# Performance work log

Hardware: AMD Instinct MI355X
Metric: run time of the kernel (lower is better)

The kernel has to match this reference:

```python
import jax, jax.numpy as jnp
import numpy as np

VOCAB, EMBED, ENC, DEC, ATT = 10000, 256, 2048, 512, 512
B, P, T = 64, 49, 30


def setup_inputs() -> dict:
    key = jax.random.key(0)
    ks = jax.random.split(key, 20)
    s = 0.02
    emb = jax.random.normal(ks[0], (VOCAB, EMBED), jnp.float32) * s
    emb = emb.at[0].set(0.0)  # padding_idx=0
    inp = {
        'features': jax.random.normal(ks[1], (B, P, ENC), jnp.float32),
        'captions': jax.random.randint(ks[2], (B, T), 0, VOCAB),
        'emb': emb,
        'W1': jax.random.normal(ks[3], (ATT, ENC), jnp.float32) * s,
        'b1': jnp.zeros((ATT,), jnp.float32),
        'W2': jax.random.normal(ks[4], (ATT, DEC), jnp.float32) * s,
        'b2': jnp.zeros((ATT,), jnp.float32),
        'V': jax.random.normal(ks[5], (1, ATT), jnp.float32) * s,
        'bV': jnp.zeros((1,), jnp.float32),
        'W_ih1': jax.random.normal(ks[6], (4 * DEC, EMBED + ENC), jnp.float32) * s,
        'W_hh1': jax.random.normal(ks[7], (4 * DEC, DEC), jnp.float32) * s,
        'b_ih1': jnp.zeros((4 * DEC,), jnp.float32),
        'b_hh1': jnp.zeros((4 * DEC,), jnp.float32),
        'W_ih2': jax.random.normal(ks[8], (4 * DEC, DEC), jnp.float32) * s,
        'W_hh2': jax.random.normal(ks[9], (4 * DEC, DEC), jnp.float32) * s,
        'b_ih2': jnp.zeros((4 * DEC,), jnp.float32),
        'b_hh2': jnp.zeros((4 * DEC,), jnp.float32),
        'fc_W': jax.random.normal(ks[10], (VOCAB, DEC), jnp.float32) * s,
        'fc_b': jnp.zeros((VOCAB,), jnp.float32),
    }
    return inp


def _lstm_cell(x, h, c, Wih, Whh, bih, bhh):
    g = x @ Wih.T + bih + h @ Whh.T + bhh  # [B, 4D]
    i, f, gg, o = jnp.split(g, 4, axis=-1)  # PyTorch gate order i,f,g,o
    c_new = jax.nn.sigmoid(f) * c + jax.nn.sigmoid(i) * jnp.tanh(gg)
    h_new = jax.nn.sigmoid(o) * jnp.tanh(c_new)
    return h_new, c_new


def reference(features, captions, emb, W1, b1, W2, b2, V, bV,
              W_ih1, W_hh1, b_ih1, b_hh1, W_ih2, W_hh2, b_ih2, b_hh2,
              fc_W, fc_b):
    # dropout is identity (eval mode / deterministic reference)
    batch = features.shape[0]
    dec = W_hh1.shape[1]
    feat_W1 = jnp.einsum('bpe,ae->bpa', features, W1) + b1  # precompute W1(features)
    embs = emb[captions]  # [B, T, E]

    def step(carry, x_t):
        h1, c1, h2, c2 = carry
        # Bahdanau attention with hidden state h2
        att = jnp.tanh(feat_W1 + (h2 @ W2.T + b2)[:, None, :])  # [B, P, A]
        score = att @ V.T + bV  # [B, P, 1]
        w = jax.nn.softmax(score, axis=1)
        ctx = jnp.sum(w * features, axis=1)  # [B, ENC]
        lstm_in = jnp.concatenate([x_t, ctx], axis=1)
        h1n, c1n = _lstm_cell(lstm_in, h1, c1, W_ih1, W_hh1, b_ih1, b_hh1)
        h2n, c2n = _lstm_cell(h1n, h2, c2, W_ih2, W_hh2, b_ih2, b_hh2)
        out = h2n @ fc_W.T + fc_b  # [B, V]
        return (h1n, c1n, h2n, c2n), out

    init = tuple(jnp.zeros((batch, dec), features.dtype) for _ in range(4))
    _, outs = jax.lax.scan(step, init, jnp.swapaxes(embs, 0, 1))  # [T, B, V]
    return jnp.swapaxes(outs, 0, 1)  # [B, T, V]
```

## Files before the change

kernel.cpp:

```cpp
#include <hip/hip_runtime.h>
#include <math.h>

#define VOCAB 10000
#define VPAD  10240
#define EMBED 256
#define ENC   2048
#define DEC   512
#define ATT   512
#define B_    64
#define P_    49
#define T_    30
#define G4    2048
#define SL    32768

typedef __bf16 bf16_t;
typedef bf16_t bf16x8 __attribute__((ext_vector_type(8)));
typedef float  f32x4  __attribute__((ext_vector_type(4)));

__device__ __forceinline__ float sigf(float x) { return 1.f / (1.f + expf(-x)); }

__global__ void prep_k(
    const float* __restrict__ b_ih1, const float* __restrict__ b_hh1, float* __restrict__ bsum1,
    const float* __restrict__ b_ih2, const float* __restrict__ b_hh2, float* __restrict__ bsum2,
    const float* __restrict__ W2,    bf16_t* __restrict__ W2sp,
    const float* __restrict__ W_hh1, bf16_t* __restrict__ fp1h,
    const float* __restrict__ W_ih2, const float* __restrict__ W_hh2, bf16_t* __restrict__ fp2,
    const float* __restrict__ fc_W,  bf16_t* __restrict__ fcWb,
    const int* __restrict__ caps, const float* __restrict__ emb, bf16_t* __restrict__ xgb,
    bf16_t* __restrict__ h1s0, bf16_t* __restrict__ h2s0,
    float* __restrict__ c1s0, float* __restrict__ c2s0,
    float* __restrict__ hwp, float* __restrict__ G1h)
{
    long stride = (long)gridDim.x * blockDim.x;
    long i0 = (long)blockIdx.x * blockDim.x + threadIdx.x;
    for (long i = i0; i < SL; i += stride) {
        h1s0[i] = (bf16_t)0.f; h2s0[i] = (bf16_t)0.f;
        c1s0[i] = 0.f; c2s0[i] = 0.f;
    }
    for (long i = i0; i < 32L * SL; i += stride) hwp[i] = 0.f;
    for (long i = i0; i < 64L * 2048; i += stride) G1h[i] = 0.f;
    for (long i = i0; i < 2048; i += stride) {
        bsum1[i] = b_ih1[i] + b_hh1[i];
        bsum2[i] = b_ih2[i] + b_hh2[i];
    }
    for (long i = i0; i < 32L * 32 * 64 * 8; i += stride) {
        long j8 = i & 7, lq = (i >> 3) & 63, nt = (i >> 9) & 31, nb = i >> 14;
        long k = (lq >> 4) * 8 + j8;
        long a = nt * 16 + (lq & 15);
        W2sp[i] = (bf16_t)(k < 16 ? W2[a * 512 + nb * 16 + k] : 0.f);
    }
    for (long i = i0; i < 32L * 16 * 2048; i += stride) {
        long j8 = i & 7, lq = (i >> 3) & 63, s = (i >> 9) & 3, nk = i >> 11;
        long kf = nk & 15, nb = nk >> 4;
        long c = s * 512 + nb * 16 + (lq & 15);
        long k = kf * 32 + (lq >> 4) * 8 + j8;
        fp1h[i] = (bf16_t)W_hh1[c * 512 + k];
    }
    for (long i = i0; i < 2048L * 1024; i += stride) {
        long j8 = i & 7, lq = (i >> 3) & 63, s = (i >> 9) & 3, nk = i >> 11;
        long kf = nk & 31, nb = nk >> 5;
        long c = s * 512 + nb * 16 + (lq & 15);
        long k = kf * 32 + (lq >> 4) * 8 + j8;
        fp2[i] = (bf16_t)(k < 512 ? W_ih2[c * 512 + k] : W_hh2[c * 512 + (k - 512)]);
    }
    for (long i = i0; i < (long)VPAD * 512; i += stride) {
        long r = i >> 9;
        fcWb[i] = (bf16_t)(r < VOCAB ? fc_W[i] : 0.f);
    }
    for (long i = i0; i < 1920L * 256; i += stride) {
        long row = i >> 8, e = i & 255;
        long tq = row >> 6, b = row & 63;
        int cap = caps[b * T_ + tq];
        xgb[i] = (bf16_t)emb[(long)cap * 256 + e];
    }
}

__global__ __launch_bounds__(256) void mm3_k(
    const float* __restrict__ features, const bf16_t* __restrict__ xgb,
    const float* __restrict__ W1, const float* __restrict__ W_ih1,
    const float* __restrict__ b1, const float* __restrict__ bsum1,
    bf16_t* __restrict__ fW1b, bf16_t* __restrict__ xembb, bf16_t* __restrict__ F1g)
{
    int bid = blockIdx.x;
    const float* Af; const bf16_t* Ab = nullptr; int lda;
    const float* Bw; int ldb, boff;
    const float* bias; bf16_t* outB; int ldo, K, bn, bm;
    if (bid < 392) {
        Af = features; lda = ENC; Bw = W1; ldb = ENC; boff = 0;
        bias = b1; outB = fW1b; ldo = ATT; K = ENC;
        bn = (bid & 7) * 64; bm = (bid >> 3) * 64;
    } else if (bid < 1352) {
        int b2i = bid - 392;
        Af = nullptr; Ab = xgb; lda = EMBED; Bw = W_ih1; ldb = EMBED + ENC; boff = 0;
        bias = bsum1; outB = xembb; ldo = G4; K = EMBED;
        bn = (b2i & 31) * 64; bm = (b2i >> 5) * 64;
    } else {
        int b3i = bid - 1352;
        Af = features; lda = ENC; Bw = W_ih1; ldb = EMBED + ENC; boff = EMBED;
        bias = nullptr; outB = F1g; ldo = G4; K = ENC;
        bn = (b3i & 31) * 64; bm = (b3i >> 5) * 64;
    }

    __shared__ bf16_t Apad[64][72];
    __shared__ bf16_t Bpad[64][72];
    const int tid = threadIdx.x;
    const int w = tid >> 6, l = tid & 63;
    f32x4 acc[4] = {};

    for (int k0 = 0; k0 < K; k0 += 64) {
        for (int c = tid; c < 512; c += 256) {
            int row = c >> 3, q = c & 7;
            if (Af) {
                const float* as = &Af[(size_t)(bm + row) * lda + k0 + q * 8];
                float4 f0 = *(const float4*)as;
                float4 f1 = *(const float4*)(as + 4);
                bf16x8 v;
                v[0] = (bf16_t)f0.x; v[1] = (bf16_t)f0.y; v[2] = (bf16_t)f0.z; v[3] = (bf16_t)f0.w;
                v[4] = (bf16_t)f1.x; v[5] = (bf16_t)f1.y; v[6] = (bf16_t)f1.z; v[7] = (bf16_t)f1.w;
                *(bf16x8*)&Apad[row][q * 8] = v;
            } else {
                *(bf16x8*)&Apad[row][q * 8] = *(const bf16x8*)&Ab[(size_t)(bm + row) * lda + k0 + q * 8];
            }
            const float* bs = &Bw[(size_t)(bn + row) * ldb + boff + k0 + q * 8];
            float4 f0 = *(const float4*)bs;
            float4 f1 = *(const float4*)(bs + 4);
            bf16x8 v;
            v[0] = (bf16_t)f0.x; v[1] = (bf16_t)f0.y; v[2] = (bf16_t)f0.z; v[3] = (bf16_t)f0.w;
            v[4] = (bf16_t)f1.x; v[5] = (bf16_t)f1.y; v[6] = (bf16_t)f1.z; v[7] = (bf16_t)f1.w;
            *(bf16x8*)&Bpad[row][q * 8] = v;
        }
        __syncthreads();
#pragma unroll
        for (int ks = 0; ks < 2; ++ks) {
            bf16x8 a8 = *(const bf16x8*)&Apad[w * 16 + (l & 15)][ks * 32 + (l >> 4) * 8];
#pragma unroll
            for (int nf = 0; nf < 4; ++nf) {
                bf16x8 b8 = *(const bf16x8*)&Bpad[nf * 16 + (l & 15)][ks * 32 + (l >> 4) * 8];
                acc[nf] = __builtin_amdgcn_mfma_f32_16x16x32_bf16(a8, b8, acc[nf], 0, 0, 0);
            }
        }
        __syncthreads();
    }

    int rbase = bm + w * 16 + (l >> 4) * 4;
    int cl = l & 15;
#pragma unroll
    for (int nf = 0; nf < 4; ++nf) {
        int col = bn + nf * 16 + cl;
        float bv = bias ? bias[col] : 0.f;
#pragma unroll
        for (int j = 0; j < 4; ++j)
            outB[(size_t)(rbase + j) * ldo + col] = (bf16_t)(acc[nf][j] + bv);
    }
}

__global__ __launch_bounds__(256) void mm_fc(
    const bf16_t* __restrict__ A, int lda,
    const bf16_t* __restrict__ Bw, int ldb,
    const float* __restrict__ bias,
    float* __restrict__ outF, int ldo, int N, int K)
{
    __shared__ bf16_t Apad[64][72];
    __shared__ bf16_t Bpad[64][72];
    const int bn = blockIdx.x * 64, bm = blockIdx.y * 64;
    const int tid = threadIdx.x;
    const int w = tid >> 6, l = tid & 63;
    f32x4 acc[4] = {};

    for (int k0 = 0; k0 < K; k0 += 64) {
        for (int c = tid; c < 512; c += 256) {
            int row = c >> 3, q = c & 7;
            *(bf16x8*)&Apad[row][q * 8] = *(const bf16x8*)&A[(size_t)(bm + row) * lda + k0 + q * 8];
            *(bf16x8*)&Bpad[row][q * 8] = *(const bf16x8*)&Bw[(size_t)(bn + row) * ldb + k0 + q * 8];
        }
        __syncthreads();
#pragma unroll
        for (int ks = 0; ks < 2; ++ks) {
            bf16x8 a8 = *(const bf16x8*)&Apad[w * 16 + (l & 15)][ks * 32 + (l >> 4) * 8];
#pragma unroll
            for (int nf = 0; nf < 4; ++nf) {
                bf16x8 b8 = *(const bf16x8*)&Bpad[nf * 16 + (l & 15)][ks * 32 + (l >> 4) * 8];
                acc[nf] = __builtin_amdgcn_mfma_f32_16x16x32_bf16(a8, b8, acc[nf], 0, 0, 0);
            }
        }
        __syncthreads();
    }

    int rbase = bm + w * 16 + (l >> 4) * 4;
    int cl = l & 15;
#pragma unroll
    for (int nf = 0; nf < 4; ++nf) {
        int col = bn + nf * 16 + cl;
#pragma unroll
        for (int j = 0; j < 4; ++j) {
            int row = rbase + j;
            if (col < N) {
                int orow = (row & 63) * T_ + (row >> 6);
                outF[(size_t)orow * ldo + col] = acc[nf][j] + bias[col];
            }
        }
    }
}

__global__ __launch_bounds__(512) void attn1_k(
    const float* __restrict__ hwp, const float* __restrict__ b2,
    const bf16_t* __restrict__ fW1b, const float* __restrict__ V,
    const float* __restrict__ bV, const bf16_t* __restrict__ F1g,
    const bf16_t* __restrict__ xeb, const float* __restrict__ G1h,
    const float* __restrict__ c1r, float* __restrict__ c1w,
    bf16_t* __restrict__ h1w)
{
    const int b = blockIdx.x, tid = threadIdx.x;
    const int w = tid >> 6, l = tid & 63;
    __shared__ float hw[512];
    __shared__ float sc[64];
    __shared__ float wn[64];
    __shared__ float gsum[2][2048];

    {
        float a0 = b2[tid];
        const float* hp = hwp + (size_t)b * 16384 + tid;
#pragma unroll 8
        for (int nb = 0; nb < 32; ++nb) a0 += hp[nb * 512];
        hw[tid] = a0;
    }
    __syncthreads();
    {
        float hwr[8], Vr[8];
#pragma unroll
        for (int i = 0; i < 8; ++i) { hwr[i] = hw[l * 8 + i]; Vr[i] = V[l * 8 + i]; }
        for (int pq = w; pq < P_; pq += 8) {
            bf16x8 f8 = *(const bf16x8*)&fW1b[(size_t)(b * P_ + pq) * 512 + l * 8];
            float s = 0.f;
#pragma unroll
            for (int i = 0; i < 8; ++i) s += tanhf((float)f8[i] + hwr[i]) * Vr[i];
#pragma unroll
            for (int o = 32; o; o >>= 1) s += __shfl_xor(s, o);
            if (l == 0) sc[pq] = s + bV[0];
        }
    }
    __syncthreads();
    {
        float m = -1e30f;
        for (int q = 0; q < P_; ++q) m = fmaxf(m, sc[q]);
        float ss = 0.f;
        for (int q = 0; q < P_; ++q) ss += expf(sc[q] - m);
        if (tid < P_) wn[tid] = expf(sc[tid] - m) / ss;
    }
    __syncthreads();
    {
        const int h = tid >> 8, th = tid & 255;
        const int p0 = h ? 25 : 0, pn = h ? 24 : 25;
        float acc[8] = {};
        const bf16_t* fg = F1g + ((size_t)b * P_ + p0) * 2048 + th * 8;
        for (int q = 0; q < pn; ++q) {
            bf16x8 f8 = *(const bf16x8*)&fg[(size_t)q * 2048];
            float wq = wn[p0 + q];
#pragma unroll
            for (int i = 0; i < 8; ++i) acc[i] += wq * (float)f8[i];
        }
#pragma unroll
        for (int i = 0; i < 8; ++i) gsum[h][th * 8 + i] = acc[i];
    }
    __syncthreads();
    {
        const int d = tid;
        const bf16_t* xb = xeb + (size_t)b * G4;
        const float* gh = G1h + b * 2048;
        float gi = (float)xb[d]        + gsum[0][d]        + gsum[1][d]        + gh[d];
        float gf = (float)xb[512 + d]  + gsum[0][512 + d]  + gsum[1][512 + d]  + gh[512 + d];
        float gg = (float)xb[1024 + d] + gsum[0][1024 + d] + gsum[1][1024 + d] + gh[1024 + d];
        float go = (float)xb[1536 + d] + gsum[0][1536 + d] + gsum[1][1536 + d] + gh[1536 + d];
        int idx = b * 512 + d;
        float cn = sigf(gf) * c1r[idx] + sigf(gi) * tanhf(gg);
        c1w[idx] = cn;
        h1w[idx] = (bf16_t)(sigf(go) * tanhf(cn));
    }
}

__global__ __launch_bounds__(512) void gate2_k(
    const bf16_t* __restrict__ h1n, const bf16_t* __restrict__ h2r,
    const bf16_t* __restrict__ fp2, const bf16_t* __restrict__ fp1h,
    const bf16_t* __restrict__ W2sp, const float* __restrict__ bsum2,
    const float* __restrict__ c2r, float* __restrict__ c2w,
    bf16_t* __restrict__ h2w, float* __restrict__ G1h, float* __restrict__ hwp)
{
    const int bid = blockIdx.x, tid = threadIdx.x;
    const int w = tid >> 6, l = tid & 63;
    const int l15 = l & 15, koff = (l >> 4) * 8;
    const int mt = w & 3, kh = w >> 2;
    __shared__ float red[2][4][4][256];
    __shared__ bf16_t h2t[64 * 16];

    if (bid < 32) {
        const int nb = bid;
        {
            const int arow = mt * 16 + l15;
            const bf16_t* ap = (kh == 0 ? h1n : h2r) + arow * 512 + koff;
            const bf16_t* wp = fp2 + ((size_t)nb * 32 + kh * 16) * 2048 + l * 8;
            f32x4 acc[4] = {};
#pragma unroll
            for (int kf = 0; kf < 16; ++kf) {
                bf16x8 a8 = *(const bf16x8*)&ap[kf * 32];
                const bf16_t* wk = wp + (size_t)kf * 2048;
#pragma unroll
                for (int s = 0; s < 4; ++s) {
                    bf16x8 w8 = *(const bf16x8*)&wk[s * 512];
                    acc[s] = __builtin_amdgcn_mfma_f32_16x16x32_bf16(a8, w8, acc[s], 0, 0, 0);
                }
            }
#pragma unroll
            for (int s = 0; s < 4; ++s) *(f32x4*)&red[kh][mt][s][l * 4] = acc[s];
        }
        __syncthreads();
        if (w < 4) {
            const int d = nb * 16 + l15;
            const int rb = w * 16 + ((l >> 4) << 2);
            f32x4 v[4];
#pragma unroll
            for (int s = 0; s < 4; ++s)
                v[s] = *(const f32x4*)&red[0][w][s][l * 4] + *(const f32x4*)&red[1][w][s][l * 4];
#pragma unroll
            for (int j = 0; j < 4; ++j) {
                int row = rb + j;
                float gi = v[0][j] + bsum2[d];
                float gf = v[1][j] + bsum2[512 + d];
                float gg = v[2][j] + bsum2[1024 + d];
                float go = v[3][j] + bsum2[1536 + d];
                float cn = sigf(gf) * c2r[row * 512 + d] + sigf(gi) * tanhf(gg);
                c2w[row * 512 + d] = cn;
                bf16_t hb = (bf16_t)(sigf(go) * tanhf(cn));
                h2w[row * 512 + d] = hb;
                h2t[row * 16 + l15] = hb;
            }
        }
        __syncthreads();
        {
            bf16x8 a8 = {};
            if ((l >> 4) < 2) a8 = *(const bf16x8*)&h2t[(mt * 16 + l15) * 16 + koff];
            const int row0 = mt * 16 + (l >> 4) * 4;
            for (int q = 0; q < 16; ++q) {
                int nt = kh * 16 + q;
                bf16x8 b8 = *(const bf16x8*)&W2sp[((size_t)(nb * 32 + nt) * 64 + l) * 8];
                f32x4 acc2 = {};
                acc2 = __builtin_amdgcn_mfma_f32_16x16x32_bf16(a8, b8, acc2, 0, 0, 0);
                const int col = nt * 16 + l15;
#pragma unroll
                for (int j = 0; j < 4; ++j)
                    hwp[(size_t)(row0 + j) * 16384 + nb * 512 + col] = acc2[j];
            }
        }
    } else {
        const int nb = bid - 32;
        {
            const int arow = mt * 16 + l15;
            const bf16_t* ap = h1n + arow * 512 + kh * 256 + koff;
            const bf16_t* wp = fp1h + ((size_t)nb * 16 + kh * 8) * 2048 + l * 8;
            f32x4 acc[4] = {};
#pragma unroll
            for (int kf = 0; kf < 8; ++kf) {
                bf16x8 a8 = *(const bf16x8*)&ap[kf * 32];
                const bf16_t* wk = wp + (size_t)kf * 2048;
#pragma unroll
                for (int s = 0; s < 4; ++s) {
                    bf16x8 w8 = *(const bf16x8*)&wk[s * 512];
                    acc[s] = __builtin_amdgcn_mfma_f32_16x16x32_bf16(a8, w8, acc[s], 0, 0, 0);
                }
            }
#pragma unroll
            for (int s = 0; s < 4; ++s) *(f32x4*)&red[kh][mt][s][l * 4] = acc[s];
        }
        __syncthreads();
        if (w < 4) {
            const int d = nb * 16 + l15;
            const int rb = w * 16 + ((l >> 4) << 2);
#pragma unroll
            for (int s = 0; s < 4; ++s) {
                f32x4 v = *(const f32x4*)&red[0][w][s][l * 4] + *(const f32x4*)&red[1][w][s][l * 4];
#pragma unroll
                for (int j = 0; j < 4; ++j)
                    G1h[(rb + j) * 2048 + s * 512 + d] = v[j];
            }
        }
    }
}

extern "C" void kernel_launch(void* const* d_in, const int* in_sizes, int n_in,
                              void* d_out, int out_size, void* d_ws, size_t ws_size,
                              hipStream_t stream)
{
    const float* features = (const float*)d_in[0];
    const int*   captions = (const int*)d_in[1];
    const float* emb   = (const float*)d_in[2];
    const float* W1    = (const float*)d_in[3];
    const float* b1    = (const float*)d_in[4];
    const float* W2    = (const float*)d_in[5];
    const float* b2    = (const float*)d_in[6];
    const float* V     = (const float*)d_in[7];
    const float* bV    = (const float*)d_in[8];
    const float* W_ih1 = (const float*)d_in[9];
    const float* W_hh1 = (const float*)d_in[10];
    const float* b_ih1 = (const float*)d_in[11];
    const float* b_hh1 = (const float*)d_in[12];
    const float* W_ih2 = (const float*)d_in[13];
    const float* W_hh2 = (const float*)d_in[14];
    const float* b_ih2 = (const float*)d_in[15];
    const float* b_hh2 = (const float*)d_in[16];
    const float* fc_W  = (const float*)d_in[17];
    const float* fc_b  = (const float*)d_in[18];
    float* out = (float*)d_out;

    char* ws = (char*)d_ws;
    size_t off = 0;
    auto alloc = [&](size_t nbytes) {
        char* pp = ws + off;
        off = (off + nbytes + 255) & ~(size_t)255;
        return pp;
    };
    bf16_t* fW1b   = (bf16_t*)alloc(3136L * 512 * 2);
    bf16_t* F1g    = (bf16_t*)alloc(3136L * 2048 * 2);
    bf16_t* W2sp   = (bf16_t*)alloc(32L * 32 * 64 * 8 * 2);
    bf16_t* fp1h   = (bf16_t*)alloc(32L * 16 * 2048 * 2);
    bf16_t* fp2    = (bf16_t*)alloc(2048L * 1024 * 2);
    bf16_t* fcWb   = (bf16_t*)alloc((size_t)VPAD * 512 * 2);
    bf16_t* xgb    = (bf16_t*)alloc(1920L * 256 * 2);
    bf16_t* xembb  = (bf16_t*)alloc(1920L * 2048 * 2);
    float*  bsum1  = (float*)alloc(2048 * 4);
    float*  bsum2  = (float*)alloc(2048 * 4);
    float*  hwp    = (float*)alloc(32L * SL * 4);
    float*  G1h    = (float*)alloc(64L * 2048 * 4);
    bf16_t* h1s    = (bf16_t*)alloc((size_t)(T_ + 1) * SL * 2);
    bf16_t* h2s    = (bf16_t*)alloc((size_t)(T_ + 1) * SL * 2);
    float*  c1s    = (float*)alloc(2L * SL * 4);
    float*  c2s    = (float*)alloc(2L * SL * 4);

    prep_k<<<4096, 256, 0, stream>>>(
        b_ih1, b_hh1, bsum1, b_ih2, b_hh2, bsum2,
        W2, W2sp, W_hh1, fp1h, W_ih2, W_hh2, fp2, fc_W, fcWb,
        captions, emb, xgb,
        h1s, h2s, c1s, c2s, hwp, G1h);

    mm3_k<<<2920, 256, 0, stream>>>(
        features, xgb, W1, W_ih1, b1, bsum1, fW1b, xembb, F1g);

    for (int t = 0; t < T_; ++t) {
        attn1_k<<<B_, 512, 0, stream>>>(
            hwp, b2, fW1b, V, bV, F1g,
            xembb + (size_t)t * B_ * G4, G1h,
            c1s + (size_t)(t & 1) * SL, c1s + (size_t)((t + 1) & 1) * SL,
            h1s + (size_t)(t + 1) * SL);
        gate2_k<<<64, 512, 0, stream>>>(
            h1s + (size_t)(t + 1) * SL, h2s + (size_t)t * SL,
            fp2, fp1h, W2sp, bsum2,
            c2s + (size_t)(t & 1) * SL, c2s + (size_t)((t + 1) & 1) * SL,
            h2s + (size_t)(t + 1) * SL, G1h, hwp);
    }

    mm_fc<<<dim3(VPAD / 64, (T_ * B_) / 64), 256, 0, stream>>>(
        h2s + SL, DEC, fcWb, DEC, fc_b, out, VOCAB, VOCAB, DEC);
}
```

Baseline: 1.140 ms.

## Fuse prep and input GEMM kernels into one launch with gathered embeddings

Merges the preprocessing kernel and the three-segment input GEMM kernel into a single launch. Extra blocks beyond the GEMM tiles do the zeroing, bias sums and weight repacking. The embedding gather now happens inside the GEMM A-tile load, so the xgb buffer goes away, and the layer-1 bias sum is computed in the epilogue instead of in prep. This removes one launch and the serialization between prep and GEMM, letting the two run concurrently, at the cost of uncoalesced gathered embedding loads.

Measured after the change: 1.146 ms. No clear change (+0.5%).

```diff
diff --git a/kernel.cpp b/kernel.cpp
--- a/kernel.cpp
+++ b/kernel.cpp
@@ -12,6 +12,8 @@
 #define T_    30
 #define G4    2048
 #define SL    32768
+#define NGEMM 2920
+#define NPREP 1080
 
 typedef __bf16 bf16_t;
 typedef bf16_t bf16x8 __attribute__((ext_vector_type(8)));
@@ -19,107 +21,101 @@
 
 __device__ __forceinline__ float sigf(float x) { return 1.f / (1.f + expf(-x)); }
 
-__global__ void prep_k(
-    const float* __restrict__ b_ih1, const float* __restrict__ b_hh1, float* __restrict__ bsum1,
-    const float* __restrict__ b_ih2, const float* __restrict__ b_hh2, float* __restrict__ bsum2,
-    const float* __restrict__ W2,    bf16_t* __restrict__ W2sp,
-    const float* __restrict__ W_hh1, bf16_t* __restrict__ fp1h,
-    const float* __restrict__ W_ih2, const float* __restrict__ W_hh2, bf16_t* __restrict__ fp2,
-    const float* __restrict__ fc_W,  bf16_t* __restrict__ fcWb,
-    const int* __restrict__ caps, const float* __restrict__ emb, bf16_t* __restrict__ xgb,
-    bf16_t* __restrict__ h1s0, bf16_t* __restrict__ h2s0,
-    float* __restrict__ c1s0, float* __restrict__ c2s0,
-    float* __restrict__ hwp, float* __restrict__ G1h)
+struct MegaP {
+    const float *features, *emb, *W1, *b1, *W2, *W_ih1, *W_hh1, *W_ih2, *W_hh2;
+    const float *b_ih1, *b_hh1, *b_ih2, *b_hh2, *fc_W;
+    const int* caps;
+    bf16_t *fW1b, *xembb, *F1g, *W2sp, *fp1h, *fp2, *fcWb;
+    float *bsum2, *hwp, *G1h, *c1s0, *c2s0;
+    bf16_t *h1s0, *h2s0;
+};
+
+__global__ __launch_bounds__(256) void mega_k(MegaP p)
 {
-    long stride = (long)gridDim.x * blockDim.x;
-    long i0 = (long)blockIdx.x * blockDim.x + threadIdx.x;
-    for (long i = i0; i < SL; i += stride) {
-        h1s0[i] = (bf16_t)0.f; h2s0[i] = (bf16_t)0.f;
-        c1s0[i] = 0.f; c2s0[i] = 0.f;
-    }
-    for (long i = i0; i < 32L * SL; i += stride) hwp[i] = 0.f;
-    for (long i = i0; i < 64L * 2048; i += stride) G1h[i] = 0.f;
-    for (long i = i0; i < 2048; i += stride) {
-        bsum1[i] = b_ih1[i] + b_hh1[i];
-        bsum2[i] = b_ih2[i] + b_hh2[i];
-    }
-    for (long i = i0; i < 32L * 32 * 64 * 8; i += stride) {
-        long j8 = i & 7, lq = (i >> 3) & 63, nt = (i >> 9) & 31, nb = i >> 14;
-        long k = (lq >> 4) * 8 + j8;
-        long a = nt * 16 + (lq & 15);
-        W2sp[i] = (bf16_t)(k < 16 ? W2[a * 512 + nb * 16 + k] : 0.f);
-    }
-    for (long i = i0; i < 32L * 16 * 2048; i += stride) {
-        long j8 = i & 7, lq = (i >> 3) & 63, s = (i >> 9) & 3, nk = i >> 11;
-        long kf = nk & 15, nb = nk >> 4;
-        long c = s * 512 + nb * 16 + (lq & 15);
-        long k = kf * 32 + (lq >> 4) * 8 + j8;
-        fp1h[i] = (bf16_t)W_hh1[c * 512 + k];
-    }
-    for (long i = i0; i < 2048L * 1024; i += stride) {
-        long j8 = i & 7, lq = (i >> 3) & 63, s = (i >> 9) & 3, nk = i >> 11;
-        long kf = nk & 31, nb = nk >> 5;
-        long c = s * 512 + nb * 16 + (lq & 15);
-        long k = kf * 32 + (lq >> 4) * 8 + j8;
-        fp2[i] = (bf16_t)(k < 512 ? W_ih2[c * 512 + k] : W_hh2[c * 512 + (k - 512)]);
-    }
-    for (long i = i0; i < (long)VPAD * 512; i += stride) {
-        long r = i >> 9;
-        fcWb[i] = (bf16_t)(r < VOCAB ? fc_W[i] : 0.f);
-    }
-    for (long i = i0; i < 1920L * 256; i += stride) {
-        long row = i >> 8, e = i & 255;
-        long tq = row >> 6, b = row & 63;
-        int cap = caps[b * T_ + tq];
-        xgb[i] = (bf16_t)emb[(long)cap * 256 + e];
-    }
-}
-
-__global__ __launch_bounds__(256) void mm3_k(
-    const float* __restrict__ features, const bf16_t* __restrict__ xgb,
-    const float* __restrict__ W1, const float* __restrict__ W_ih1,
-    const float* __restrict__ b1, const float* __restrict__ bsum1,
-    bf16_t* __restrict__ fW1b, bf16_t* __restrict__ xembb, bf16_t* __restrict__ F1g)
-{
-    int bid = blockIdx.x;
-    const float* Af; const bf16_t* Ab = nullptr; int lda;
+    const int bid = blockIdx.x;
+    const int tid = threadIdx.x;
+
+    if (bid >= NGEMM) {
+        long stride = (long)NPREP * 256;
+        long i0 = (long)(bid - NGEMM) * 256 + tid;
+        for (long i = i0; i < SL; i += stride) {
+            p.h1s0[i] = (bf16_t)0.f; p.h2s0[i] = (bf16_t)0.f;
+            p.c1s0[i] = 0.f; p.c2s0[i] = 0.f;
+        }
+        for (long i = i0; i < 32L * SL; i += stride) p.hwp[i] = 0.f;
+        for (long i = i0; i < 64L * 2048; i += stride) p.G1h[i] = 0.f;
+        for (long i = i0; i < 2048; i += stride)
+            p.bsum2[i] = p.b_ih2[i] + p.b_hh2[i];
+        for (long i = i0; i < 32L * 32 * 64 * 8; i += stride) {
+            long j8 = i & 7, lq = (i >> 3) & 63, nt = (i >> 9) & 31, nb = i >> 14;
+            long k = (lq >> 4) * 8 + j8;
+            long a = nt * 16 + (lq & 15);
+            p.W2sp[i] = (bf16_t)(k < 16 ? p.W2[a * 512 + nb * 16 + k] : 0.f);
+        }
+        for (long i = i0; i < 32L * 16 * 2048; i += stride) {
+            long j8 = i & 7, lq = (i >> 3) & 63, s = (i >> 9) & 3, nk = i >> 11;
+            long kf = nk & 15, nb = nk >> 4;
+            long c = s * 512 + nb * 16 + (lq & 15);
+            long k = kf * 32 + (lq >> 4) * 8 + j8;
+            p.fp1h[i] = (bf16_t)p.W_hh1[c * 512 + k];
+        }
+        for (long i = i0; i < 2048L * 1024; i += stride) {
+            long j8 = i & 7, lq = (i >> 3) & 63, s = (i >> 9) & 3, nk = i >> 11;
+            long kf = nk & 31, nb = nk >> 5;
+            long c = s * 512 + nb * 16 + (lq & 15);
+            long k = kf * 32 + (lq >> 4) * 8 + j8;
+            p.fp2[i] = (bf16_t)(k < 512 ? p.W_ih2[c * 512 + k] : p.W_hh2[c * 512 + (k - 512)]);
+        }
+        for (long i = i0; i < (long)VPAD * 512; i += stride) {
+            long r = i >> 9;
+            p.fcWb[i] = (bf16_t)(r < VOCAB ? p.fc_W[i] : 0.f);
+        }
+        return;
+    }
+
+    int seg; const float* Af; int lda;
     const float* Bw; int ldb, boff;
-    const float* bias; bf16_t* outB; int ldo, K, bn, bm;
+    bf16_t* outB; int ldo, K, bn, bm;
     if (bid < 392) {
-        Af = features; lda = ENC; Bw = W1; ldb = ENC; boff = 0;
-        bias = b1; outB = fW1b; ldo = ATT; K = ENC;
+        seg = 0; Af = p.features; lda = ENC; Bw = p.W1; ldb = ENC; boff = 0;
+        outB = p.fW1b; ldo = ATT; K = ENC;
         bn = (bid & 7) * 64; bm = (bid >> 3) * 64;
     } else if (bid < 1352) {
         int b2i = bid - 392;
-        Af = nullptr; Ab = xgb; lda = EMBED; Bw = W_ih1; ldb = EMBED + ENC; boff = 0;
-        bias = bsum1; outB = xembb; ldo = G4; K = EMBED;
+        seg = 1; Af = nullptr; lda = 0; Bw = p.W_ih1; ldb = EMBED + ENC; boff = 0;
+        outB = p.xembb; ldo = G4; K = EMBED;
         bn = (b2i & 31) * 64; bm = (b2i >> 5) * 64;
     } else {
         int b3i = bid - 1352;
-        Af = features; lda = ENC; Bw = W_ih1; ldb = EMBED + ENC; boff = EMBED;
-        bias = nullptr; outB = F1g; ldo = G4; K = ENC;
+        seg = 2; Af = p.features; lda = ENC; Bw = p.W_ih1; ldb = EMBED + ENC; boff = EMBED;
+        outB = p.F1g; ldo = G4; K = ENC;
         bn = (b3i & 31) * 64; bm = (b3i >> 5) * 64;
     }
 
     __shared__ bf16_t Apad[64][72];
     __shared__ bf16_t Bpad[64][72];
-    const int tid = threadIdx.x;
     const int w = tid >> 6, l = tid & 63;
     f32x4 acc[4] = {};
 
     for (int k0 = 0; k0 < K; k0 += 64) {
         for (int c = tid; c < 512; c += 256) {
             int row = c >> 3, q = c & 7;
-            if (Af) {
-                const float* as = &Af[(size_t)(bm + row) * lda + k0 + q * 8];
+            const float* as;
+            if (seg == 1) {
+                int m = bm + row;
+                int tq = m >> 6, b = m & 63;
+                int cap = p.caps[b * T_ + tq];
+                as = &p.emb[(size_t)cap * 256 + k0 + q * 8];
+            } else {
+                as = &Af[(size_t)(bm + row) * lda + k0 + q * 8];
+            }
+            {
                 float4 f0 = *(const float4*)as;
                 float4 f1 = *(const float4*)(as + 4);
                 bf16x8 v;
                 v[0] = (bf16_t)f0.x; v[1] = (bf16_t)f0.y; v[2] = (bf16_t)f0.z; v[3] = (bf16_t)f0.w;
                 v[4] = (bf16_t)f1.x; v[5] = (bf16_t)f1.y; v[6] = (bf16_t)f1.z; v[7] = (bf16_t)f1.w;
                 *(bf16x8*)&Apad[row][q * 8] = v;
-            } else {
-                *(bf16x8*)&Apad[row][q * 8] = *(const bf16x8*)&Ab[(size_t)(bm + row) * lda + k0 + q * 8];
             }
             const float* bs = &Bw[(size_t)(bn + row) * ldb + boff + k0 + q * 8];
             float4 f0 = *(const float4*)bs;
@@ -147,7 +143,8 @@
 #pragma unroll
     for (int nf = 0; nf < 4; ++nf) {
         int col = bn + nf * 16 + cl;
-        float bv = bias ? bias[col] : 0.f;
+        float bv = (seg == 0) ? p.b1[col]
+                 : (seg == 1) ? (p.b_ih1[col] + p.b_hh1[col]) : 0.f;
 #pragma unroll
         for (int j = 0; j < 4; ++j)
             outB[(size_t)(rbase + j) * ldo + col] = (bf16_t)(acc[nf][j] + bv);
@@ -423,9 +420,7 @@
     bf16_t* fp1h   = (bf16_t*)alloc(32L * 16 * 2048 * 2);
     bf16_t* fp2    = (bf16_t*)alloc(2048L * 1024 * 2);
     bf16_t* fcWb   = (bf16_t*)alloc((size_t)VPAD * 512 * 2);
-    bf16_t* xgb    = (bf16_t*)alloc(1920L * 256 * 2);
     bf16_t* xembb  = (bf16_t*)alloc(1920L * 2048 * 2);
-    float*  bsum1  = (float*)alloc(2048 * 4);
     float*  bsum2  = (float*)alloc(2048 * 4);
     float*  hwp    = (float*)alloc(32L * SL * 4);
     float*  G1h    = (float*)alloc(64L * 2048 * 4);
@@ -434,14 +429,17 @@
     float*  c1s    = (float*)alloc(2L * SL * 4);
     float*  c2s    = (float*)alloc(2L * SL * 4);
 
-    prep_k<<<4096, 256, 0, stream>>>(
-        b_ih1, b_hh1, bsum1, b_ih2, b_hh2, bsum2,
-        W2, W2sp, W_hh1, fp1h, W_ih2, W_hh2, fp2, fc_W, fcWb,
-        captions, emb, xgb,
-        h1s, h2s, c1s, c2s, hwp, G1h);
-
-    mm3_k<<<2920, 256, 0, stream>>>(
-        features, xgb, W1, W_ih1, b1, bsum1, fW1b, xembb, F1g);
+    MegaP mp;
+    mp.features = features; mp.emb = emb; mp.W1 = W1; mp.b1 = b1; mp.W2 = W2;
+    mp.W_ih1 = W_ih1; mp.W_hh1 = W_hh1; mp.W_ih2 = W_ih2; mp.W_hh2 = W_hh2;
+    mp.b_ih1 = b_ih1; mp.b_hh1 = b_hh1; mp.b_ih2 = b_ih2; mp.b_hh2 = b_hh2;
+    mp.fc_W = fc_W; mp.caps = captions;
+    mp.fW1b = fW1b; mp.xembb = xembb; mp.F1g = F1g; mp.W2sp = W2sp;
+    mp.fp1h = fp1h; mp.fp2 = fp2; mp.fcWb = fcWb;
+    mp.bsum2 = bsum2; mp.hwp = hwp; mp.G1h = G1h;
+    mp.c1s0 = c1s; mp.c2s0 = c2s; mp.h1s0 = h1s; mp.h2s0 = h2s;
+
+    mega_k<<<NGEMM + NPREP, 256, 0, stream>>>(mp);
 
     for (int t = 0; t < T_; ++t) {
         attn1_k<<<B_, 512, 0, stream>>>(
```
